# Kernel optimization log

Hardware: AMD Instinct MI355X
Metric: run time of the kernel (lower is better)

The kernel has to match this reference:

```python
import jax, jax.numpy as jnp
import numpy as np

EPS_LN = 1e-5
EPS_BN = 1e-5
NUM_HEADS = 8


def _gelu(x):
    return jax.nn.gelu(x, approximate=False)


def _ln(x, w, b):
    # LayerNorm over last (channel) dim, eps=1e-5 (torch default)
    mu = jnp.mean(x, axis=-1, keepdims=True)
    var = jnp.mean((x - mu) ** 2, axis=-1, keepdims=True)
    return (x - mu) / jnp.sqrt(var + EPS_LN) * w + b


def _bn(x, g, b):
    # eval-mode BatchNorm2d on NCHW with running_mean=0, running_var=1
    scale = g * (1.0 + EPS_BN) ** -0.5
    return x * scale[None, :, None, None] + b[None, :, None, None]


def _conv1x1(x, w):
    # x: [B,C,H,W], w: [O,C]
    return jnp.einsum('bchw,oc->bohw', x, w)


def _unfold3(x, r):
    # nn.Unfold(kernel=3, dilation=r, padding=r): gather 3x3 dilated neighborhoods
    B, C, H, W = x.shape
    xp = jnp.pad(x, ((0, 0), (0, 0), (r, r), (r, r)))
    pats = [xp[:, :, i * r:i * r + H, j * r:j * r + W] for i in range(3) for j in range(3)]
    return jnp.stack(pats, axis=2)  # [B,C,9,H,W]


def _atrous_attn(q, k, v, num_heads, r):
    # per-pixel local attention: q [B,C,H,W] attends to 9 dilated neighbors of k/v
    B, C, H, W = q.shape
    hd = C // num_heads
    scale = hd ** -0.5
    qh = q.reshape(B, num_heads, hd, H, W)
    kp = _unfold3(k, r).reshape(B, num_heads, hd, 9, H, W)
    attn = jax.nn.softmax(jnp.einsum('bnchw,bnckhw->bnkhw', qh, kp) * scale, axis=2)
    vp = _unfold3(v, r).reshape(B, num_heads, hd, 9, H, W)
    out = jnp.einsum('bnkhw,bnckhw->bnchw', attn, vp)
    return out.reshape(B, C, H, W).transpose(0, 2, 3, 1)  # [B,H,W,C]


def _window_attn(x_bhwc, qkv_w, proj_w, proj_b, num_heads, r):
    xc = x_bhwc.transpose(0, 3, 1, 2)
    C = xc.shape[1]
    qkv = _conv1x1(xc, qkv_w)  # [B,3C,H,W], order q|k|v
    out = _atrous_attn(qkv[:, :C], qkv[:, C:2 * C], qkv[:, 2 * C:], num_heads, r)
    return jnp.einsum('bhwc,oc->bhwo', out, proj_w) + proj_b


def _mlp(x_bhwc, c1_w, c1_b, bn1_g, bn1_b, dw_w, dw_b, bn2_g, bn2_b, c2_w, c2_b, bn3_g, bn3_b):
    xc = x_bhwc.transpose(0, 3, 1, 2)
    h = _bn(_gelu(_conv1x1(xc, c1_w) + c1_b[None, :, None, None]), bn1_g, bn1_b)
    dw = jax.lax.conv_general_dilated(h, dw_w, (1, 1), 'SAME',
                                      feature_group_count=h.shape[1],
                                      dimension_numbers=('NCHW', 'OIHW', 'NCHW'))
    dw = dw + dw_b[None, :, None, None]
    h = _bn(_gelu(dw + h), bn2_g, bn2_b)
    out = _bn(_conv1x1(h, c2_w) + c2_b[None, :, None, None], bn3_g, bn3_b)
    return out.transpose(0, 2, 3, 1)


def reference(x, ln1_w, ln1_b, ln2_w, ln2_b,
              qkv1_w, proj1_w, proj1_b, qkv2_w, proj2_w, proj2_b, qkv3_w, proj3_w, proj3_b,
              tc_conv_w, tc_conv_b, tc_bn1_g, tc_bn1_b, tc_pool_w, tc_bn2_g, tc_bn2_b,
              tc_trans_w, tc_trans_b, tc_bn3_g, tc_bn3_b,
              mlp_c1_w, mlp_c1_b, mlp_bn1_g, mlp_bn1_b, mlp_dw_w, mlp_dw_b,
              mlp_bn2_g, mlp_bn2_b, mlp_c2_w, mlp_c2_b, mlp_bn3_g, mlp_bn3_b):
    tx = x.transpose(0, 2, 3, 1)  # [B,H,W,C]
    n1 = _ln(tx, ln1_w, ln1_b)
    t1 = tx + _window_attn(n1, qkv1_w, proj1_w, proj1_b, NUM_HEADS, 1)
    t2 = tx + _window_attn(n1, qkv2_w, proj2_w, proj2_b, NUM_HEADS, 2)
    t3 = tx + _window_attn(n1, qkv3_w, proj3_w, proj3_b, NUM_HEADS, 3)
    # Trans_conv: ASPP-style fusion
    xc1 = jax.nn.relu(_bn(_conv1x1(x, tc_conv_w) + tc_conv_b[None, :, None, None], tc_bn1_g, tc_bn1_b))
    pool = jnp.mean(x, axis=(2, 3), keepdims=True)
    pool = jax.nn.relu(_bn(_conv1x1(pool, tc_pool_w), tc_bn2_g, tc_bn2_b))
    pool = jnp.broadcast_to(pool, x.shape)  # bilinear upsample of a 1x1 map == broadcast
    cat = jnp.concatenate([xc1, t1.transpose(0, 3, 1, 2), t2.transpose(0, 3, 1, 2),
                           t3.transpose(0, 3, 1, 2), pool], axis=1)  # [B,5C,H,W]
    tr = jax.nn.relu(_bn(_conv1x1(cat, tc_trans_w) + tc_trans_b[None, :, None, None],
                         tc_bn3_g, tc_bn3_b)).transpose(0, 2, 3, 1)  # [B,H,W,C]
    tr = tr + _mlp(_ln(tr, ln2_w, ln2_b), mlp_c1_w, mlp_c1_b, mlp_bn1_g, mlp_bn1_b,
                   mlp_dw_w, mlp_dw_b, mlp_bn2_g, mlp_bn2_b, mlp_c2_w, mlp_c2_b,
                   mlp_bn3_g, mlp_bn3_b)
    return tr.transpose(0, 3, 1, 2)  # [B,C,H,W]


def setup_inputs():
    key = jax.random.key(0)
    B, C, H, W = 4, 256, 64, 64
    HID = 4 * C
    ks = iter(jax.random.split(key, 64))

    def nrm(shape, scale=0.02):
        return jax.random.normal(next(ks), shape, dtype=jnp.float32) * scale

    inp = {
        'x': jax.random.normal(next(ks), (B, C, H, W), dtype=jnp.float32),
        'ln1_w': jnp.ones((C,), jnp.float32), 'ln1_b': jnp.zeros((C,), jnp.float32),
        'ln2_w': jnp.ones((C,), jnp.float32), 'ln2_b': jnp.zeros((C,), jnp.float32),
    }
    for i in (1, 2, 3):
        inp[f'qkv{i}_w'] = nrm((3 * C, C))
        inp[f'proj{i}_w'] = nrm((C, C))
        inp[f'proj{i}_b'] = jnp.zeros((C,), jnp.float32)
    inp.update(
        tc_conv_w=nrm((C, C)), tc_conv_b=jnp.zeros((C,), jnp.float32),
        tc_bn1_g=jnp.ones((C,), jnp.float32), tc_bn1_b=jnp.zeros((C,), jnp.float32),
        tc_pool_w=nrm((C, C)),
        tc_bn2_g=jnp.ones((C,), jnp.float32), tc_bn2_b=jnp.zeros((C,), jnp.float32),
        tc_trans_w=nrm((C, 5 * C)), tc_trans_b=jnp.zeros((C,), jnp.float32),
        tc_bn3_g=jnp.ones((C,), jnp.float32), tc_bn3_b=jnp.zeros((C,), jnp.float32),
        mlp_c1_w=nrm((HID, C)), mlp_c1_b=jnp.zeros((HID,), jnp.float32),
        mlp_bn1_g=jnp.ones((HID,), jnp.float32), mlp_bn1_b=jnp.zeros((HID,), jnp.float32),
        mlp_dw_w=nrm((HID, 1, 3, 3), 0.1), mlp_dw_b=jnp.zeros((HID,), jnp.float32),
        mlp_bn2_g=jnp.ones((HID,), jnp.float32), mlp_bn2_b=jnp.zeros((HID,), jnp.float32),
        mlp_c2_w=nrm((C, HID)), mlp_c2_b=jnp.zeros((C,), jnp.float32),
        mlp_bn3_g=jnp.ones((C,), jnp.float32), mlp_bn3_b=jnp.zeros((C,), jnp.float32),
    )
    return inp
```

## Files before the change

kernel.cpp:

```cpp
#include <hip/hip_runtime.h>

#define N_PIX 16384
#define CDIM  256
#define HIDD  1024
#define BNS   0.9999950000374997f
#define LP    36

typedef __attribute__((ext_vector_type(8))) short  short8;
typedef __attribute__((ext_vector_type(4))) float  f32x4;
typedef __attribute__((ext_vector_type(4))) int    int4v;
typedef __attribute__((ext_vector_type(2))) int    int2v;

__device__ __forceinline__ float b2f(unsigned short u){
  unsigned int x = ((unsigned int)u) << 16; float f;
  __builtin_memcpy(&f, &x, 4); return f;
}
__device__ __forceinline__ unsigned short f2b(float f){
  unsigned int x; __builtin_memcpy(&x, &f, 4);
  unsigned int r = (x + 0x7fffu + ((x >> 16) & 1u)) >> 16;
  return (unsigned short)r;
}
__device__ __forceinline__ float geluf(float x){
  return 0.5f * x * (1.0f + erff(x * 0.70710678118654752f));
}

__global__ __launch_bounds__(256) void k_cvt(const float* __restrict__ src,
                                             unsigned short* __restrict__ dst, int n){
  int i = (blockIdx.x * 256 + threadIdx.x) * 8;
  if (i >= n) return;
  f32x4 a = *(const f32x4*)(src + i);
  f32x4 b = *(const f32x4*)(src + i + 4);
  unsigned short o[8];
  #pragma unroll
  for (int j = 0; j < 4; ++j){ o[j] = f2b(a[j]); o[4 + j] = f2b(b[j]); }
  *(int4v*)(dst + i) = *(int4v*)o;
}

__global__ __launch_bounds__(256) void k_dwwT(const float* __restrict__ dww,
                                              unsigned short* __restrict__ dwwT){
  int i = blockIdx.x * 256 + threadIdx.x;
  if (i >= 9216) return;
  int kk = i >> 10, c = i & 1023;
  dwwT[i] = f2b(dww[c * 9 + kk]);
}

__global__ __launch_bounds__(256) void k_transpose(const float* __restrict__ x,
                                                   unsigned short* __restrict__ xpm,
                                                   float* __restrict__ xpm32){
  __shared__ __align__(16) float tile[64][65];
  int b = blockIdx.z, c0 = blockIdx.y * 64, p0 = blockIdx.x * 64;
  int t = threadIdx.x;
  int r = t >> 3, k = t & 7;
  for (int s = 0; s < 2; ++s){
    int rr = r + s * 32;
    const float* src = x + (((size_t)(b * CDIM + c0 + rr)) << 12) + p0 + k * 8;
    f32x4 a = *(const f32x4*)src;
    f32x4 c = *(const f32x4*)(src + 4);
    #pragma unroll
    for (int j = 0; j < 4; ++j){ tile[rr][k * 8 + j] = a[j]; tile[rr][k * 8 + 4 + j] = c[j]; }
  }
  __syncthreads();
  for (int s = 0; s < 2; ++s){
    int pr = r + s * 32;
    float tf[8];
    unsigned short tb[8];
    #pragma unroll
    for (int j = 0; j < 8; ++j){ tf[j] = tile[k * 8 + j][pr]; tb[j] = f2b(tf[j]); }
    size_t rowoff = ((size_t)(b * 4096 + p0 + pr)) << 8;
    *(int4v*)(xpm + rowoff + c0 + k * 8) = *(int4v*)tb;
    *(f32x4*)(xpm32 + rowoff + c0 + k * 8)     = *(f32x4*)&tf[0];
    *(f32x4*)(xpm32 + rowoff + c0 + k * 8 + 4) = *(f32x4*)&tf[4];
  }
}

template<typename IT>
__global__ __launch_bounds__(256) void k_ln(const IT* __restrict__ in,
    const float* __restrict__ w, const float* __restrict__ bia,
    unsigned short* __restrict__ out){
  int row  = blockIdx.x * 4 + (threadIdx.x >> 6);
  int lane = threadIdx.x & 63;
  float v[4];
  const IT* p = in + (size_t)row * CDIM + lane * 4;
  if constexpr (sizeof(IT) == 2){
    int2v d = *(const int2v*)p;
    unsigned short tmp[4]; __builtin_memcpy(tmp, &d, 8);
    #pragma unroll
    for (int j = 0; j < 4; ++j) v[j] = b2f(tmp[j]);
  } else {
    f32x4 d = *(const f32x4*)p;
    #pragma unroll
    for (int j = 0; j < 4; ++j) v[j] = d[j];
  }
  float s  = v[0] + v[1] + v[2] + v[3];
  float s2 = v[0]*v[0] + v[1]*v[1] + v[2]*v[2] + v[3]*v[3];
  #pragma unroll
  for (int m = 1; m < 64; m <<= 1){
    s  += __shfl_xor(s,  m);
    s2 += __shfl_xor(s2, m);
  }
  float mu   = s * (1.0f / 256.0f);
  float var  = s2 * (1.0f / 256.0f) - mu * mu;
  float rstd = rsqrtf(var + 1e-5f);
  unsigned short o[4];
  #pragma unroll
  for (int j = 0; j < 4; ++j){
    int c = lane * 4 + j;
    o[j] = f2b((v[j] - mu) * rstd * w[c] + bia[c]);
  }
  *(int2v*)(out + (size_t)row * CDIM + lane * 4) = *(int2v*)o;
}

template<int MODE>
__global__ __launch_bounds__(256) void k_gemm(
    const unsigned short* __restrict__ A, const unsigned short* __restrict__ Bw,
    int K, int Nout, int ldb, void* __restrict__ outp,
    const float* __restrict__ bias,
    const float* __restrict__ bng,
    const float* __restrict__ bnb,
    const float* __restrict__ auxf,
    int catoff)
{
  __shared__ __align__(16) unsigned short As[64][LP];
  __shared__ __align__(16) unsigned short Bs[128][LP];
  int t = threadIdx.x;
  int m0 = blockIdx.y * 64, n0 = blockIdx.x * 128;
  int wave = t >> 6, lane = t & 63;
  int wm = wave >> 1, wn = wave & 1;
  int lr = lane & 15, kb = lane >> 4;

  f32x4 acc[2][4];
  f32x4 z = {0.f, 0.f, 0.f, 0.f};
  #pragma unroll
  for (int i = 0; i < 2; ++i)
    #pragma unroll
    for (int j = 0; j < 4; ++j) acc[i][j] = z;

  int r = t >> 2, cc = t & 3;
  for (int k0 = 0; k0 < K; k0 += 32){
    *(int4v*)&As[r][cc * 8]      = *(const int4v*)&A [(size_t)(m0 + r) * K        + k0 + cc * 8];
    *(int4v*)&Bs[r][cc * 8]      = *(const int4v*)&Bw[(size_t)(n0 + r) * ldb      + k0 + cc * 8];
    *(int4v*)&Bs[r + 64][cc * 8] = *(const int4v*)&Bw[(size_t)(n0 + r + 64) * ldb + k0 + cc * 8];
    __syncthreads();
    short8 af[2], bf_[4];
    #pragma unroll
    for (int i = 0; i < 2; ++i) af [i] = *(const short8*)&As[wm * 32 + i * 16 + lr][kb * 8];
    #pragma unroll
    for (int j = 0; j < 4; ++j) bf_[j] = *(const short8*)&Bs[wn * 64 + j * 16 + lr][kb * 8];
    #pragma unroll
    for (int i = 0; i < 2; ++i)
      #pragma unroll
      for (int j = 0; j < 4; ++j)
        acc[i][j] = __builtin_amdgcn_mfma_f32_16x16x32_bf16(af[i], bf_[j], acc[i][j], 0, 0, 0);
    __syncthreads();
  }

  #pragma unroll
  for (int i = 0; i < 2; ++i){
    int rowb = m0 + wm * 32 + i * 16 + kb * 4;
    #pragma unroll
    for (int j = 0; j < 4; ++j){
      int col = n0 + wn * 64 + j * 16 + lr;
      #pragma unroll
      for (int rr = 0; rr < 4; ++rr){
        int row = rowb + rr;
        float v = acc[i][j][rr];
        if constexpr (MODE == 0){
          ((unsigned short*)outp)[(size_t)row * Nout + col] = f2b(v);
        } else if constexpr (MODE == 1){
          v += bias[col] + auxf[(size_t)row * CDIM + col];
          ((unsigned short*)outp)[(size_t)row * HIDD + catoff + col] = f2b(v);
        } else if constexpr (MODE == 2){
          v = (v + bias[col]) * (bng[col] * BNS) + bnb[col];
          v = fmaxf(v, 0.0f);
          ((unsigned short*)outp)[(size_t)row * HIDD + col] = f2b(v);
        } else if constexpr (MODE == 3){
          v += bias[col] + auxf[((row >> 12) << 8) + col];
          v = v * (bng[col] * BNS) + bnb[col];
          v = fmaxf(v, 0.0f);
          ((float*)outp)[(size_t)row * CDIM + col] = v;
        } else if constexpr (MODE == 4){
          v = geluf(v + bias[col]);
          v = v * (bng[col] * BNS) + bnb[col];
          ((unsigned short*)outp)[(size_t)row * HIDD + col] = f2b(v);
        } else {
          v = (v + bias[col]) * (bng[col] * BNS) + bnb[col];
          v += auxf[(size_t)row * CDIM + col];
          int b = row >> 12, hw = row & 4095;
          ((float*)outp)[(((size_t)(b * CDIM + col)) << 12) + hw] = v;
        }
      }
    }
  }
}

__global__ __launch_bounds__(256) void k_attn(const unsigned short* __restrict__ QKV,
                                              unsigned short* __restrict__ ATT, int r){
  int t = blockIdx.x * 256 + threadIdx.x;
  int head = t & 7, pix = t >> 3;
  int hw = pix & 4095, h = hw >> 6, w = hw & 63;
  const unsigned short* base = QKV + (size_t)pix * 768 + head * 32;

  float q[32];
  #pragma unroll
  for (int c8 = 0; c8 < 4; ++c8){
    int4v d = *(const int4v*)(base + c8 * 8);
    unsigned short tmp[8]; __builtin_memcpy(tmp, &d, 16);
    #pragma unroll
    for (int j = 0; j < 8; ++j) q[c8 * 8 + j] = b2f(tmp[j]);
  }
  float logit[9];
  #pragma unroll
  for (int jj = 0; jj < 9; ++jj){
    int dh = (jj / 3 - 1) * r, dw = (jj % 3 - 1) * r;
    int hh = h + dh, ww = w + dw;
    float d = 0.0f;
    if (hh >= 0 && hh < 64 && ww >= 0 && ww < 64){
      const unsigned short* kr = base + (dh * 64 + dw) * 768 + 256;
      #pragma unroll
      for (int c8 = 0; c8 < 4; ++c8){
        int4v dd = *(const int4v*)(kr + c8 * 8);
        unsigned short tmp[8]; __builtin_memcpy(tmp, &dd, 16);
        #pragma unroll
        for (int j = 0; j < 8; ++j) d += q[c8 * 8 + j] * b2f(tmp[j]);
      }
    }
    logit[jj] = d * 0.17677669529663687f;
  }
  float m = logit[0];
  #pragma unroll
  for (int jj = 1; jj < 9; ++jj) m = fmaxf(m, logit[jj]);
  float p[9], s = 0.0f;
  #pragma unroll
  for (int jj = 0; jj < 9; ++jj){ p[jj] = __expf(logit[jj] - m); s += p[jj]; }
  float inv = 1.0f / s;
  float o[32];
  #pragma unroll
  for (int j = 0; j < 32; ++j) o[j] = 0.0f;
  #pragma unroll
  for (int jj = 0; jj < 9; ++jj){
    int dh = (jj / 3 - 1) * r, dw = (jj % 3 - 1) * r;
    int hh = h + dh, ww = w + dw;
    if (hh >= 0 && hh < 64 && ww >= 0 && ww < 64){
      float pj = p[jj] * inv;
      const unsigned short* vr = base + (dh * 64 + dw) * 768 + 512;
      #pragma unroll
      for (int c8 = 0; c8 < 4; ++c8){
        int4v dd = *(const int4v*)(vr + c8 * 8);
        unsigned short tmp[8]; __builtin_memcpy(tmp, &dd, 16);
        #pragma unroll
        for (int j = 0; j < 8; ++j) o[c8 * 8 + j] += pj * b2f(tmp[j]);
      }
    }
  }
  unsigned short ob[32];
  #pragma unroll
  for (int j = 0; j < 32; ++j) ob[j] = f2b(o[j]);
  unsigned short* op = ATT + (size_t)pix * CDIM + head * 32;
  #pragma unroll
  for (int c8 = 0; c8 < 4; ++c8) *(int4v*)(op + c8 * 8) = *(int4v*)&ob[c8 * 8];
}

__global__ __launch_bounds__(256) void k_dwconv(const unsigned short* __restrict__ H,
    const unsigned short* __restrict__ dwwT, const float* __restrict__ dwb,
    const float* __restrict__ g, const float* __restrict__ bb,
    unsigned short* __restrict__ H2){
  int t = blockIdx.x * 256 + threadIdx.x;
  int chunk = t & 127, pix = t >> 7;
  int hw = pix & 4095, h = hw >> 6, w = hw & 63;
  int c0 = chunk * 8;
  float acc[8], hc[8];
  {
    int4v dd = *(const int4v*)(H + (size_t)pix * HIDD + c0);
    unsigned short tmp[8]; __builtin_memcpy(tmp, &dd, 16);
    #pragma unroll
    for (int j = 0; j < 8; ++j){ hc[j] = b2f(tmp[j]); acc[j] = 0.0f; }
  }
  #pragma unroll
  for (int di = -1; di <= 1; ++di)
    #pragma unroll
    for (int dj = -1; dj <= 1; ++dj){
      int hh = h + di, ww = w + dj;
      if (hh < 0 || hh >= 64 || ww < 0 || ww >= 64) continue;
      int kk = (di + 1) * 3 + (dj + 1);
      int4v dd = *(const int4v*)(H + ((size_t)(pix + di * 64 + dj)) * HIDD + c0);
      int4v wv = *(const int4v*)(dwwT + kk * 1024 + c0);
      unsigned short tmp[8], wt[8];
      __builtin_memcpy(tmp, &dd, 16);
      __builtin_memcpy(wt,  &wv, 16);
      #pragma unroll
      for (int j = 0; j < 8; ++j) acc[j] += b2f(wt[j]) * b2f(tmp[j]);
    }
  f32x4 bv0 = *(const f32x4*)(dwb + c0), bv1 = *(const f32x4*)(dwb + c0 + 4);
  f32x4 gv0 = *(const f32x4*)(g   + c0), gv1 = *(const f32x4*)(g   + c0 + 4);
  f32x4 cv0 = *(const f32x4*)(bb  + c0), cv1 = *(const f32x4*)(bb  + c0 + 4);
  float bvv[8], gvv[8], cvv[8];
  #pragma unroll
  for (int j = 0; j < 4; ++j){
    bvv[j] = bv0[j]; bvv[4 + j] = bv1[j];
    gvv[j] = gv0[j]; gvv[4 + j] = gv1[j];
    cvv[j] = cv0[j]; cvv[4 + j] = cv1[j];
  }
  unsigned short ob[8];
  #pragma unroll
  for (int j = 0; j < 8; ++j){
    float v = acc[j] + bvv[j] + hc[j];
    v = geluf(v);
    v = v * (gvv[j] * BNS) + cvv[j];
    ob[j] = f2b(v);
  }
  *(int4v*)(H2 + (size_t)pix * HIDD + c0) = *(int4v*)ob;
}

__global__ __launch_bounds__(256) void k_pool_mean(const float* __restrict__ x,
                                                   float* __restrict__ pm){
  int bc = blockIdx.x;
  const float* p = x + ((size_t)bc << 12);
  int t = threadIdx.x;
  float s = 0.0f;
  for (int i = t * 4; i < 4096; i += 1024){
    f32x4 dd = *(const f32x4*)(p + i);
    s += dd[0] + dd[1] + dd[2] + dd[3];
  }
  #pragma unroll
  for (int m = 1; m < 64; m <<= 1) s += __shfl_xor(s, m);
  __shared__ float red[4];
  if ((t & 63) == 0) red[t >> 6] = s;
  __syncthreads();
  if (t == 0) pm[bc] = (red[0] + red[1] + red[2] + red[3]) * (1.0f / 4096.0f);
}

__global__ __launch_bounds__(256) void k_pool_feat(const float* __restrict__ pm,
    const float* __restrict__ pw, const float* __restrict__ g,
    const float* __restrict__ bb, float* __restrict__ pf){
  int b = blockIdx.x, o = threadIdx.x;
  __shared__ float v[256];
  v[o] = pm[b * 256 + o];
  __syncthreads();
  float acc = 0.0f;
  const float* wr = pw + (size_t)o * 256;
  for (int c = 0; c < 256; ++c) acc += v[c] * wr[c];
  float val = acc * (g[o] * BNS) + bb[o];
  pf[b * 256 + o] = fmaxf(val, 0.0f);
}

__global__ __launch_bounds__(256) void k_pool_bias(const float* __restrict__ pf,
    const float* __restrict__ tw, float* __restrict__ pb){
  int b = blockIdx.x, o = threadIdx.x;
  __shared__ float v[256];
  v[o] = pf[b * 256 + o];
  __syncthreads();
  float acc = 0.0f;
  const float* wr = tw + (size_t)o * 1280 + 1024;
  for (int c = 0; c < 256; ++c) acc += v[c] * wr[c];
  pb[b * 256 + o] = acc;
}

extern "C" void kernel_launch(void* const* d_in, const int* in_sizes, int n_in,
                              void* d_out, int out_size, void* d_ws, size_t ws_size,
                              hipStream_t stream){
  const float* x     = (const float*)d_in[0];
  const float* ln1w  = (const float*)d_in[1];
  const float* ln1b  = (const float*)d_in[2];
  const float* ln2w  = (const float*)d_in[3];
  const float* ln2b  = (const float*)d_in[4];
  const float* qkvw[3]  = {(const float*)d_in[5], (const float*)d_in[8],  (const float*)d_in[11]};
  const float* projw[3] = {(const float*)d_in[6], (const float*)d_in[9],  (const float*)d_in[12]};
  const float* projb[3] = {(const float*)d_in[7], (const float*)d_in[10], (const float*)d_in[13]};
  const float* tcw   = (const float*)d_in[14];
  const float* tcb   = (const float*)d_in[15];
  const float* bn1g  = (const float*)d_in[16];
  const float* bn1b  = (const float*)d_in[17];
  const float* poolw = (const float*)d_in[18];
  const float* bn2g  = (const float*)d_in[19];
  const float* bn2b  = (const float*)d_in[20];
  const float* trw   = (const float*)d_in[21];
  const float* trb   = (const float*)d_in[22];
  const float* bn3g  = (const float*)d_in[23];
  const float* bn3b  = (const float*)d_in[24];
  const float* c1w   = (const float*)d_in[25];
  const float* c1b   = (const float*)d_in[26];
  const float* mbn1g = (const float*)d_in[27];
  const float* mbn1b = (const float*)d_in[28];
  const float* dww   = (const float*)d_in[29];
  const float* dwb   = (const float*)d_in[30];
  const float* mbn2g = (const float*)d_in[31];
  const float* mbn2b = (const float*)d_in[32];
  const float* c2w   = (const float*)d_in[33];
  const float* c2b   = (const float*)d_in[34];
  const float* mbn3g = (const float*)d_in[35];
  const float* mbn3b = (const float*)d_in[36];

  char* ws = (char*)d_ws;
  unsigned short* Xpm = (unsigned short*)(ws);
  unsigned short* N1  = (unsigned short*)(ws + 8388608);
  unsigned short* CAT = (unsigned short*)(ws + 16777216);
  float*          TR  = (float*)        (ws + 50331648);
  float*          Xpm32 = TR;
  unsigned short* E   = (unsigned short*)(ws + 67108864);
  unsigned short* F   = (unsigned short*)(ws + 100663296);
  unsigned short* Wb    = (unsigned short*)(ws + 134217728);
  unsigned short* qkvb[3]  = {Wb, Wb + 196608, Wb + 393216};
  unsigned short* projbw[3] = {Wb + 589824, Wb + 655360, Wb + 720896};
  unsigned short* tcwb  = Wb + 786432;
  unsigned short* trwb  = Wb + 851968;
  unsigned short* c1wb  = Wb + 1179648;
  unsigned short* c2wb  = Wb + 1441792;
  unsigned short* dwwT  = Wb + 1703936;
  float*          pm  = (float*)(ws + 134217728 + 3428352);
  float*          pf  = pm + 1024;
  float*          pb  = pf + 1024;

  for (int i = 0; i < 3; ++i){
    k_cvt<<<96, 256, 0, stream>>>(qkvw[i], qkvb[i], 196608);
    k_cvt<<<32, 256, 0, stream>>>(projw[i], projbw[i], 65536);
  }
  k_cvt<<<32,  256, 0, stream>>>(tcw, tcwb, 65536);
  k_cvt<<<160, 256, 0, stream>>>(trw, trwb, 327680);
  k_cvt<<<128, 256, 0, stream>>>(c1w, c1wb, 262144);
  k_cvt<<<128, 256, 0, stream>>>(c2w, c2wb, 262144);
  k_dwwT<<<36, 256, 0, stream>>>(dww, dwwT);

  k_transpose<<<dim3(64, 4, 4), 256, 0, stream>>>(x, Xpm, Xpm32);
  k_pool_mean<<<1024, 256, 0, stream>>>(x, pm);
  k_ln<unsigned short><<<4096, 256, 0, stream>>>(Xpm, ln1w, ln1b, N1);
  k_pool_feat<<<4, 256, 0, stream>>>(pm, poolw, bn2g, bn2b, pf);
  k_pool_bias<<<4, 256, 0, stream>>>(pf, trw, pb);

  for (int i = 0; i < 3; ++i){
    k_gemm<0><<<dim3(6, 256), 256, 0, stream>>>(N1, qkvb[i], 256, 768, 256, E,
                                                nullptr, nullptr, nullptr, nullptr, 0);
    k_attn<<<512, 256, 0, stream>>>(E, F, i + 1);
    k_gemm<1><<<dim3(2, 256), 256, 0, stream>>>(F, projbw[i], 256, 256, 256, CAT,
                                                projb[i], nullptr, nullptr, Xpm32,
                                                (i + 1) * 256);
  }
  k_gemm<2><<<dim3(2, 256), 256, 0, stream>>>(Xpm, tcwb, 256, 256, 256, CAT,
                                              tcb, bn1g, bn1b, nullptr, 0);
  k_gemm<3><<<dim3(2, 256), 256, 0, stream>>>(CAT, trwb, 1024, 256, 1280, TR,
                                              trb, bn3g, bn3b, pb, 0);
  k_ln<float><<<4096, 256, 0, stream>>>(TR, ln2w, ln2b, N1);
  k_gemm<4><<<dim3(8, 256), 256, 0, stream>>>(N1, c1wb, 256, 1024, 256, E,
                                              c1b, mbn1g, mbn1b, nullptr, 0);
  k_dwconv<<<8192, 256, 0, stream>>>(E, dwwT, dwb, mbn2g, mbn2b, F);
  k_gemm<5><<<dim3(2, 256), 256, 0, stream>>>(F, c2wb, 1024, 256, 1024, d_out,
                                              c2b, mbn3g, mbn3b, TR, 0);
}
```

Before: 458.8 us.

## Use direct global-to-LDS loads in GEMM and merge small launches

The GEMM tile staging now uses global_load_lds, which copies 16 bytes per lane straight from global memory into shared memory. The shared tiles become unpadded 32-wide rows laid out in the order that instruction writes. Separately, the ten weight-conversion launches are merged into one 2D-grid kernel, and the two pooled-branch kernels are fused into one. This removes the VGPR round-trip for tile loads and several launch overheads. The risks are LDS bank conflicts from dropping the padding and whether the async load completes before the barrier without an explicit wait.

```diff
diff --git a/kernel.cpp b/kernel.cpp
--- a/kernel.cpp
+++ b/kernel.cpp
@@ -4,7 +4,6 @@
 #define CDIM  256
 #define HIDD  1024
 #define BNS   0.9999950000374997f
-#define LP    36
 
 typedef __attribute__((ext_vector_type(8))) short  short8;
 typedef __attribute__((ext_vector_type(4))) float  f32x4;
@@ -24,10 +23,25 @@
   return 0.5f * x * (1.0f + erff(x * 0.70710678118654752f));
 }
 
-__global__ __launch_bounds__(256) void k_cvt(const float* __restrict__ src,
-                                             unsigned short* __restrict__ dst, int n){
+typedef const __attribute__((address_space(1))) unsigned int* gas_t;
+typedef __attribute__((address_space(3))) unsigned int*       las_t;
+__device__ __forceinline__ void gload16(const void* g, void* l){
+  __builtin_amdgcn_global_load_lds((gas_t)g, (las_t)l, 16, 0, 0);
+}
+
+__global__ __launch_bounds__(256) void k_cvt_all(
+    const float* __restrict__ s0, const float* __restrict__ s1, const float* __restrict__ s2,
+    const float* __restrict__ s3, const float* __restrict__ s4, const float* __restrict__ s5,
+    const float* __restrict__ s6, const float* __restrict__ s7, const float* __restrict__ s8,
+    const float* __restrict__ s9, unsigned short* __restrict__ wb){
+  const float* srcs[10] = {s0,s1,s2,s3,s4,s5,s6,s7,s8,s9};
+  const int n[10]   = {196608,196608,196608,65536,65536,65536,65536,327680,262144,262144};
+  const int off[10] = {0,196608,393216,589824,655360,720896,786432,851968,1179648,1441792};
+  int seg = blockIdx.y;
   int i = (blockIdx.x * 256 + threadIdx.x) * 8;
-  if (i >= n) return;
+  if (i >= n[seg]) return;
+  const float* src = srcs[seg];
+  unsigned short* dst = wb + off[seg];
   f32x4 a = *(const f32x4*)(src + i);
   f32x4 b = *(const f32x4*)(src + i + 4);
   unsigned short o[8];
@@ -120,12 +134,13 @@
     const float* __restrict__ auxf,
     int catoff)
 {
-  __shared__ __align__(16) unsigned short As[64][LP];
-  __shared__ __align__(16) unsigned short Bs[128][LP];
+  __shared__ __align__(16) unsigned short As[64 * 32];
+  __shared__ __align__(16) unsigned short Bs[128 * 32];
   int t = threadIdx.x;
   int m0 = blockIdx.y * 64, n0 = blockIdx.x * 128;
-  int wave = t >> 6, lane = t & 63;
-  int wm = wave >> 1, wn = wave & 1;
+  int lane = t & 63;
+  int w  = __builtin_amdgcn_readfirstlane(t >> 6);
+  int wm = w >> 1, wn = w & 1;
   int lr = lane & 15, kb = lane >> 4;
 
   f32x4 acc[2][4];
@@ -135,17 +150,24 @@
     #pragma unroll
     for (int j = 0; j < 4; ++j) acc[i][j] = z;
 
-  int r = t >> 2, cc = t & 3;
+  int srow = lane >> 2, schunk = (lane & 3) * 8;
+  const unsigned short* gA  = A  + (size_t)(m0 + w * 16 + srow) * K   + schunk;
+  const unsigned short* gB0 = Bw + (size_t)(n0 + w * 16 + srow) * ldb + schunk;
+  const unsigned short* gB1 = Bw + (size_t)(n0 + 64 + w * 16 + srow) * ldb + schunk;
+  unsigned short* lA  = As + w * 512;
+  unsigned short* lB0 = Bs + w * 512;
+  unsigned short* lB1 = Bs + 2048 + w * 512;
+
   for (int k0 = 0; k0 < K; k0 += 32){
-    *(int4v*)&As[r][cc * 8]      = *(const int4v*)&A [(size_t)(m0 + r) * K        + k0 + cc * 8];
-    *(int4v*)&Bs[r][cc * 8]      = *(const int4v*)&Bw[(size_t)(n0 + r) * ldb      + k0 + cc * 8];
-    *(int4v*)&Bs[r + 64][cc * 8] = *(const int4v*)&Bw[(size_t)(n0 + r + 64) * ldb + k0 + cc * 8];
+    gload16(gA  + k0, lA);
+    gload16(gB0 + k0, lB0);
+    gload16(gB1 + k0, lB1);
     __syncthreads();
     short8 af[2], bf_[4];
     #pragma unroll
-    for (int i = 0; i < 2; ++i) af [i] = *(const short8*)&As[wm * 32 + i * 16 + lr][kb * 8];
-    #pragma unroll
-    for (int j = 0; j < 4; ++j) bf_[j] = *(const short8*)&Bs[wn * 64 + j * 16 + lr][kb * 8];
+    for (int i = 0; i < 2; ++i) af [i] = *(const short8*)&As[(wm * 32 + i * 16 + lr) * 32 + kb * 8];
+    #pragma unroll
+    for (int j = 0; j < 4; ++j) bf_[j] = *(const short8*)&Bs[(wn * 64 + j * 16 + lr) * 32 + kb * 8];
     #pragma unroll
     for (int i = 0; i < 2; ++i)
       #pragma unroll
@@ -329,30 +351,25 @@
   if (t == 0) pm[bc] = (red[0] + red[1] + red[2] + red[3]) * (1.0f / 4096.0f);
 }
 
-__global__ __launch_bounds__(256) void k_pool_feat(const float* __restrict__ pm,
+__global__ __launch_bounds__(256) void k_poolfb(const float* __restrict__ pm,
     const float* __restrict__ pw, const float* __restrict__ g,
-    const float* __restrict__ bb, float* __restrict__ pf){
+    const float* __restrict__ bb, const float* __restrict__ tw,
+    float* __restrict__ pb){
   int b = blockIdx.x, o = threadIdx.x;
   __shared__ float v[256];
+  __shared__ float pfs[256];
   v[o] = pm[b * 256 + o];
   __syncthreads();
   float acc = 0.0f;
   const float* wr = pw + (size_t)o * 256;
   for (int c = 0; c < 256; ++c) acc += v[c] * wr[c];
   float val = acc * (g[o] * BNS) + bb[o];
-  pf[b * 256 + o] = fmaxf(val, 0.0f);
-}
-
-__global__ __launch_bounds__(256) void k_pool_bias(const float* __restrict__ pf,
-    const float* __restrict__ tw, float* __restrict__ pb){
-  int b = blockIdx.x, o = threadIdx.x;
-  __shared__ float v[256];
-  v[o] = pf[b * 256 + o];
+  pfs[o] = fmaxf(val, 0.0f);
   __syncthreads();
-  float acc = 0.0f;
-  const float* wr = tw + (size_t)o * 1280 + 1024;
-  for (int c = 0; c < 256; ++c) acc += v[c] * wr[c];
-  pb[b * 256 + o] = acc;
+  float acc2 = 0.0f;
+  const float* tr = tw + (size_t)o * 1280 + 1024;
+  for (int c = 0; c < 256; ++c) acc2 += pfs[c] * tr[c];
+  pb[b * 256 + o] = acc2;
 }
 
 extern "C" void kernel_launch(void* const* d_in, const int* in_sizes, int n_in,
@@ -407,24 +424,17 @@
   unsigned short* c2wb  = Wb + 1441792;
   unsigned short* dwwT  = Wb + 1703936;
   float*          pm  = (float*)(ws + 134217728 + 3428352);
-  float*          pf  = pm + 1024;
-  float*          pb  = pf + 1024;
-
-  for (int i = 0; i < 3; ++i){
-    k_cvt<<<96, 256, 0, stream>>>(qkvw[i], qkvb[i], 196608);
-    k_cvt<<<32, 256, 0, stream>>>(projw[i], projbw[i], 65536);
-  }
-  k_cvt<<<32,  256, 0, stream>>>(tcw, tcwb, 65536);
-  k_cvt<<<160, 256, 0, stream>>>(trw, trwb, 327680);
-  k_cvt<<<128, 256, 0, stream>>>(c1w, c1wb, 262144);
-  k_cvt<<<128, 256, 0, stream>>>(c2w, c2wb, 262144);
+  float*          pb  = pm + 1024;
+
+  k_cvt_all<<<dim3(160, 10), 256, 0, stream>>>(qkvw[0], qkvw[1], qkvw[2],
+                                               projw[0], projw[1], projw[2],
+                                               tcw, trw, c1w, c2w, Wb);
   k_dwwT<<<36, 256, 0, stream>>>(dww, dwwT);
 
   k_transpose<<<dim3(64, 4, 4), 256, 0, stream>>>(x, Xpm, Xpm32);
   k_pool_mean<<<1024, 256, 0, stream>>>(x, pm);
   k_ln<unsigned short><<<4096, 256, 0, stream>>>(Xpm, ln1w, ln1b, N1);
-  k_pool_feat<<<4, 256, 0, stream>>>(pm, poolw, bn2g, bn2b, pf);
-  k_pool_bias<<<4, 256, 0, stream>>>(pf, trw, pb);
+  k_poolfb<<<4, 256, 0, stream>>>(pm, poolw, bn2g, bn2b, trw, pb);
 
   for (int i = 0; i < 3; ++i){
     k_gemm<0><<<dim3(6, 256), 256, 0, stream>>>(N1, qkvb[i], 256, 768, 256, E,
```

New measurement: 433.8 us. -5.4%, faster.
